# Kernel optimization log

Measured on AMD Instinct MI355X. Metric: run time of the kernel, lower is better.

## Reference

```python
import jax, jax.numpy as jnp
import numpy as np

N_NODES = 100000
N_EDGES = 1600000
F = 64          # node_features (in == out for EvolveGCNO)
HID = 64        # hidden_size


def setup_inputs() -> dict:
    key = jax.random.key(0)
    ks = jax.random.split(key, 12)
    s = 1.0 / np.sqrt(F)
    inp = {
        "x": jax.random.normal(ks[0], (N_NODES, F), dtype=jnp.float32),
        "edge_index": jax.random.randint(ks[1], (2, N_EDGES), 0, N_NODES, dtype=jnp.int64),
        "edge_weight": jax.random.uniform(ks[2], (N_EDGES,), dtype=jnp.float32),
        # evolving GCN weight (initial_weight of EvolveGCNO)
        "W0": jax.random.uniform(ks[3], (F, F), jnp.float32, -s, s),
        # GRU (input_size=F, hidden_size=F): gates ordered r, z, n
        "gru_Wi": jax.random.uniform(ks[4], (3 * F, F), jnp.float32, -s, s),
        "gru_Wh": jax.random.uniform(ks[5], (3 * F, F), jnp.float32, -s, s),
        "gru_bi": jax.random.uniform(ks[6], (3 * F,), jnp.float32, -s, s),
        "gru_bh": jax.random.uniform(ks[7], (3 * F,), jnp.float32, -s, s),
        # projection F -> HID and head HID -> 1
        "proj_W": jax.random.uniform(ks[8], (HID, F), jnp.float32, -s, s),
        "proj_b": jax.random.uniform(ks[9], (HID,), jnp.float32, -s, s),
        "lin_W": jax.random.uniform(ks[10], (1, HID), jnp.float32, -1.0 / np.sqrt(HID), 1.0 / np.sqrt(HID)),
        "lin_b": jax.random.uniform(ks[11], (1,), jnp.float32, -1.0 / np.sqrt(HID), 1.0 / np.sqrt(HID)),
    }
    return inp


def reference(x, edge_index, edge_weight, W0, gru_Wi, gru_Wh, gru_bi, gru_bh,
              proj_W, proj_b, lin_W, lin_b):
    N = x.shape[0]
    # --- EvolveGCNO weight evolution: one GRU step, rows of W0 are both input and hidden ---
    gi = W0 @ gru_Wi.T + gru_bi  # [F, 3F]
    gh = W0 @ gru_Wh.T + gru_bh  # [F, 3F]
    i_r, i_z, i_n = jnp.split(gi, 3, axis=1)
    h_r, h_z, h_n = jnp.split(gh, 3, axis=1)
    r = jax.nn.sigmoid(i_r + h_r)
    z = jax.nn.sigmoid(i_z + h_z)
    n = jnp.tanh(i_n + r * h_n)
    W = (1.0 - z) * n + z * W0  # evolved GCN weight [F, F]

    # --- GCNConv with fixed evolved W: X' = D^-1/2 (A + I) D^-1/2 (X W) ---
    xw = x @ W  # [N, F]
    src, dst = edge_index[0], edge_index[1]
    loop = jnp.arange(N)
    src2 = jnp.concatenate([src, loop])
    dst2 = jnp.concatenate([dst, loop])
    w2 = jnp.concatenate([edge_weight, jnp.ones((N,), xw.dtype)])  # self-loop weight 1
    deg = jax.ops.segment_sum(w2, dst2, num_segments=N)
    dinv = jnp.where(deg > 0, jax.lax.rsqrt(deg), 0.0)
    norm = dinv[src2] * w2 * dinv[dst2]  # [E + N]
    h = jax.ops.segment_sum(xw[src2] * norm[:, None], dst2, num_segments=N)  # [N, F]

    # --- MLP head (dropout is identity in eval) ---
    h = jax.nn.relu(h @ proj_W.T + proj_b)
    return h @ lin_W.T + lin_b  # [N, 1]
```

## Files before the change

kernel.cpp:

```cpp
#include <hip/hip_runtime.h>
#include <stdint.h>

#define FDIM 64
#define BINSH 6
#define NBINS 1563
#define BCAP 1536
#define OVCAP 8192
#define PSTAGE 8192
#define PBLK 196
#define LSTRIDE 72

__device__ __forceinline__ float bf2f(unsigned int u) {
    union { float f; uint32_t i; } v; v.i = (u & 0xFFFFu) << 16; return v.f;
}
__device__ __forceinline__ unsigned short f2bf(float f) {
    union { float f; uint32_t i; } v; v.f = f;
    uint32_t u = v.i;
    u += 0x7FFFu + ((u >> 16) & 1u);
    return (unsigned short)(u >> 16);
}

__global__ __launch_bounds__(256) void k_sentinel(float* out, int N, float val) {
    int n = blockIdx.x * 256 + threadIdx.x;
    if (n < N) out[n] = (n == 0) ? val : 0.f;
}

__global__ __launch_bounds__(1024) void k_prep(
    const int* __restrict__ src, const int* __restrict__ dst,
    const float* __restrict__ ew, int* __restrict__ gcnt,
    int2* __restrict__ part, int* __restrict__ ovf_cnt,
    int* __restrict__ ovs, int* __restrict__ ovd, float* __restrict__ ovw, int E,
    const float* __restrict__ W0, const float* __restrict__ Wi,
    const float* __restrict__ Wh, const float* __restrict__ bi,
    const float* __restrict__ bh, const float* __restrict__ projW,
    float* __restrict__ M) {
    __shared__ int2 sorted_[PSTAGE];
    __shared__ int  gposa[PSTAGE];
    __shared__ int  hist[NBINS];
    __shared__ int  lbase[NBINS];
    __shared__ int  lcur[NBINS];
    __shared__ int  gboff[NBINS];
    __shared__ int  wsum[16];
    int t = threadIdx.x;
    if (blockIdx.x < PBLK) {
        for (int b = t; b < NBINS; b += 1024) hist[b] = 0;
        __syncthreads();
        int e0 = blockIdx.x * PSTAGE;
        int cnt = E - e0; if (cnt > PSTAGE) cnt = PSTAGE;
        for (int i = t; i < cnt; i += 1024) atomicAdd(&hist[dst[e0 + i] >> BINSH], 1);
        __syncthreads();
        for (int b = t; b < NBINS; b += 1024) {
            int h = hist[b];
            gboff[b] = h ? atomicAdd(&gcnt[b], h) : 0;
        }
        int b0i = 2 * t, b1i = 2 * t + 1;
        int h0 = (b0i < NBINS) ? hist[b0i] : 0;
        int h1 = (b1i < NBINS) ? hist[b1i] : 0;
        int c2 = h0 + h1;
        int lane = t & 63, wid = t >> 6;
        int v = c2;
#pragma unroll
        for (int d = 1; d < 64; d <<= 1) {
            int o = __shfl_up(v, d);
            if (lane >= d) v += o;
        }
        if (lane == 63) wsum[wid] = v;
        __syncthreads();
        if (t < 16) {
            int w = wsum[t];
#pragma unroll
            for (int d = 1; d < 16; d <<= 1) {
                int o = __shfl_up(w, d);
                if (t >= d) w += o;
            }
            wsum[t] = w;
        }
        __syncthreads();
        int base = (wid > 0) ? wsum[wid - 1] : 0;
        int excl = base + v - c2;
        if (b0i < NBINS) { lbase[b0i] = excl;      lcur[b0i] = excl; }
        if (b1i < NBINS) { lbase[b1i] = excl + h0; lcur[b1i] = excl + h0; }
        __syncthreads();
        for (int i = t; i < cnt; i += 1024) {
            int e = e0 + i;
            int d = dst[e];
            int b = d >> BINSH;
            int p = atomicAdd(&lcur[b], 1);
            sorted_[p] = make_int2(src[e] | ((d & 63) << 20), __float_as_int(ew[e]));
            int off = gboff[b] + (p - lbase[b]);
            if (off < BCAP) {
                gposa[p] = b * BCAP + off;
            } else {
                gposa[p] = -1;
                int op = atomicAdd(ovf_cnt, 1);
                if (op < OVCAP) { ovs[op] = src[e]; ovd[op] = d; ovw[op] = ew[e]; }
            }
        }
        __syncthreads();
        for (int j = t; j < cnt; j += 1024) {
            int g = gposa[j];
            if (g >= 0) part[g] = sorted_[j];
        }
    } else {
        int i = blockIdx.x - PBLK;
        float* w0s  = (float*)sorted_;
        float* wrow = w0s + 64;
        if (t < 64) w0s[t] = W0[i * 64 + t];
        __syncthreads();
        if (t < 64) {
            int j = t;
            float a0 = 0.f, a1 = 0.f, a2 = 0.f, b0 = 0.f, b1 = 0.f, b2 = 0.f;
#pragma unroll 8
            for (int k = 0; k < 64; k++) {
                float w0k = w0s[k];
                a0 += w0k * Wi[(j)       * 64 + k];
                a1 += w0k * Wi[(64 + j)  * 64 + k];
                a2 += w0k * Wi[(128 + j) * 64 + k];
                b0 += w0k * Wh[(j)       * 64 + k];
                b1 += w0k * Wh[(64 + j)  * 64 + k];
                b2 += w0k * Wh[(128 + j) * 64 + k];
            }
            float ir = a0 + bi[j],        hr = b0 + bh[j];
            float iz = a1 + bi[64 + j],   hz = b1 + bh[64 + j];
            float in_ = a2 + bi[128 + j], hn = b2 + bh[128 + j];
            float r = 1.f / (1.f + expf(-(ir + hr)));
            float z = 1.f / (1.f + expf(-(iz + hz)));
            float n = tanhf(in_ + r * hn);
            wrow[j] = (1.f - z) * n + z * w0s[j];
        }
        __syncthreads();
        if (t < 64) {
            float s = 0.f;
#pragma unroll 8
            for (int q = 0; q < 64; q++) s += wrow[q] * projW[t * 64 + q];
            M[i * 64 + t] = s;
        }
    }
}

__global__ __launch_bounds__(256) void k_xmdeg(
    const float* __restrict__ x, const float* __restrict__ M,
    unsigned short* __restrict__ xm, int N,
    const int* __restrict__ gcnt, const int2* __restrict__ part,
    const int* __restrict__ ovf_cnt, const int* __restrict__ ovd,
    const float* __restrict__ ovw, float* __restrict__ dinv,
    int* __restrict__ loffg) {
    __shared__ char sm[34816];
    int t = threadIdx.x;
    if (blockIdx.x < NBINS) {
        float* xs = (float*)sm;
        float* ms = xs + 64 * 68;
        int nb = blockIdx.x * 64;
#pragma unroll
        for (int i = 0; i < 4; i++) {
            int lin = i * 1024 + t * 4;
            int row = lin >> 6, col = lin & 63;
            int node = nb + row;
            float4 v = make_float4(0.f, 0.f, 0.f, 0.f);
            if (node < N) v = *(const float4*)(x + (size_t)node * 64 + col);
            *(float4*)&xs[row * 68 + col] = v;
            *(float4*)&ms[row * 68 + col] = *(const float4*)(M + lin);
        }
        __syncthreads();
        int tj = t & 15, tn = t >> 4;
        float acc[4][4] = {};
        for (int k = 0; k < 64; k += 4) {
            float4 xv[4], mv[4];
#pragma unroll
            for (int nn = 0; nn < 4; nn++) xv[nn] = *(const float4*)&xs[(tn * 4 + nn) * 68 + k];
#pragma unroll
            for (int kk = 0; kk < 4; kk++) mv[kk] = *(const float4*)&ms[(k + kk) * 68 + tj * 4];
#pragma unroll
            for (int nn = 0; nn < 4; nn++) {
                const float* xp = (const float*)&xv[nn];
#pragma unroll
                for (int kk = 0; kk < 4; kk++) {
                    float xk = xp[kk];
                    const float* mp = (const float*)&mv[kk];
                    acc[nn][0] += xk * mp[0];
                    acc[nn][1] += xk * mp[1];
                    acc[nn][2] += xk * mp[2];
                    acc[nn][3] += xk * mp[3];
                }
            }
        }
#pragma unroll
        for (int nn = 0; nn < 4; nn++) {
            int node = nb + tn * 4 + nn;
            if (node < N) {
                ushort4 o;
                o.x = f2bf(acc[nn][0]); o.y = f2bf(acc[nn][1]);
                o.z = f2bf(acc[nn][2]); o.w = f2bf(acc[nn][3]);
                *(ushort4*)&xm[(size_t)node * 64 + tj * 4] = o;
            }
        }
    } else {
        int b = blockIdx.x - NBINS;
        float* dl   = (float*)sm;
        int*   cntl = (int*)(dl + 64);
        int*   lofl = cntl + 64;
        if (t < 64) { dl[t] = 1.0f; cntl[t] = 0; }
        __syncthreads();
        int c = gcnt[b]; if (c > BCAP) c = BCAP;
        const int2* pe = part + (size_t)b * BCAP;
        for (int i = t; i < c; i += 256) {
            int2 e = pe[i];
            int nl = (e.x >> 20) & 63;
            atomicAdd(&dl[nl], __int_as_float(e.y));
            atomicAdd(&cntl[nl], 1);
        }
        int m = *ovf_cnt; if (m > OVCAP) m = OVCAP;
        for (int i = t; i < m; i += 256) {
            int d = ovd[i];
            if ((d >> BINSH) == b) atomicAdd(&dl[d & 63], ovw[i]);
        }
        __syncthreads();
        if (t == 0) {
            int o = 0;
#pragma unroll 16
            for (int k = 0; k < 64; k++) { lofl[k] = o; o += cntl[k]; }
            lofl[64] = o;
        }
        __syncthreads();
        if (t < 64) {
            int n = b * 64 + t;
            if (n < N) dinv[n] = rsqrtf(dl[t]);
        }
        if (t < 65) loffg[b * LSTRIDE + t] = lofl[t];
    }
}

__global__ __launch_bounds__(256) void k_gf(
    const unsigned short* __restrict__ xm, const float* __restrict__ dinv,
    const int* __restrict__ gcnt, const int2* __restrict__ part,
    const int* __restrict__ loffg,
    const float* __restrict__ projB, const float* __restrict__ linW,
    const float* __restrict__ linB, const int* __restrict__ ovf_cnt,
    const int* __restrict__ ovs, const int* __restrict__ ovd,
    const float* __restrict__ ovw, float* __restrict__ out, int N) {
    __shared__ int  loff[65];
    __shared__ int  lcur[32];
    __shared__ int2 ledge[BCAP];
    __shared__ float pbs[64], lws[64];
    int t = threadIdx.x, hb = blockIdx.x;
    int b = hb >> 1, half = hb & 1, nl0 = half << 5;
    if (t < 65) loff[t] = loffg[b * LSTRIDE + t];
    if (t < 64) { pbs[t] = projB[t]; lws[t] = linW[t]; }
    __syncthreads();
    int base = loff[nl0];
    if (t < 32) lcur[t] = loff[nl0 + t] - base;
    __syncthreads();
    int c = gcnt[b]; if (c > BCAP) c = BCAP;
    const int2* pe = part + (size_t)b * BCAP;
    for (int i = t; i < c; i += 256) {
        int2 e = pe[i];
        int nl = (e.x >> 20) & 63;
        if ((nl >> 5) != half) continue;
        int s = e.x & 0xFFFFF;
        float nw = dinv[s] * __int_as_float(e.y);
        int p = atomicAdd(&lcur[nl & 31], 1);
        ledge[p] = make_int2(e.x, __float_as_int(nw));
    }
    __syncthreads();
    int m = *ovf_cnt; if (m > OVCAP) m = OVCAP;
    float lb = linB[0];
    int wv = t >> 6, lane = t & 63, eg = lane >> 4, fq = lane & 15, f = fq * 4;
    for (int j = wv; j < 32; j += 4) {
        int nl = nl0 + j;
        int n = b * 64 + nl;
        if (n >= N) continue;
        float dn = dinv[n];
        int beg = loff[nl] - base, end = loff[nl + 1] - base;
        float a0 = 0.f, a1 = 0.f, a2 = 0.f, a3 = 0.f;
        float b0 = 0.f, b1 = 0.f, b2 = 0.f, b3 = 0.f;
        float c0 = 0.f, c1 = 0.f, c2 = 0.f, c3 = 0.f;
        float d0 = 0.f, d1 = 0.f, d2 = 0.f, d3 = 0.f;
        int i = beg + eg;
        for (; i + 12 < end; i += 16) {
            int2 e0 = ledge[i];
            int2 e1 = ledge[i + 4];
            int2 e2 = ledge[i + 8];
            int2 e3 = ledge[i + 12];
            uint2 u0 = *(const uint2*)&xm[(size_t)(e0.x & 0xFFFFF) * 64 + f];
            uint2 u1 = *(const uint2*)&xm[(size_t)(e1.x & 0xFFFFF) * 64 + f];
            uint2 u2 = *(const uint2*)&xm[(size_t)(e2.x & 0xFFFFF) * 64 + f];
            uint2 u3 = *(const uint2*)&xm[(size_t)(e3.x & 0xFFFFF) * 64 + f];
            float w0 = __int_as_float(e0.y);
            float w1 = __int_as_float(e1.y);
            float w2 = __int_as_float(e2.y);
            float w3 = __int_as_float(e3.y);
            a0 += w0 * bf2f(u0.x); a1 += w0 * bf2f(u0.x >> 16);
            a2 += w0 * bf2f(u0.y); a3 += w0 * bf2f(u0.y >> 16);
            b0 += w1 * bf2f(u1.x); b1 += w1 * bf2f(u1.x >> 16);
            b2 += w1 * bf2f(u1.y); b3 += w1 * bf2f(u1.y >> 16);
            c0 += w2 * bf2f(u2.x); c1 += w2 * bf2f(u2.x >> 16);
            c2 += w2 * bf2f(u2.y); c3 += w2 * bf2f(u2.y >> 16);
            d0 += w3 * bf2f(u3.x); d1 += w3 * bf2f(u3.x >> 16);
            d2 += w3 * bf2f(u3.y); d3 += w3 * bf2f(u3.y >> 16);
        }
        for (; i + 4 < end; i += 8) {
            int2 e0 = ledge[i];
            int2 e1 = ledge[i + 4];
            uint2 u0 = *(const uint2*)&xm[(size_t)(e0.x & 0xFFFFF) * 64 + f];
            uint2 u1 = *(const uint2*)&xm[(size_t)(e1.x & 0xFFFFF) * 64 + f];
            float w0 = __int_as_float(e0.y);
            float w1 = __int_as_float(e1.y);
            a0 += w0 * bf2f(u0.x); a1 += w0 * bf2f(u0.x >> 16);
            a2 += w0 * bf2f(u0.y); a3 += w0 * bf2f(u0.y >> 16);
            b0 += w1 * bf2f(u1.x); b1 += w1 * bf2f(u1.x >> 16);
            b2 += w1 * bf2f(u1.y); b3 += w1 * bf2f(u1.y >> 16);
        }
        for (; i < end; i += 4) {
            int2 e0 = ledge[i];
            uint2 u0 = *(const uint2*)&xm[(size_t)(e0.x & 0xFFFFF) * 64 + f];
            float w0 = __int_as_float(e0.y);
            a0 += w0 * bf2f(u0.x); a1 += w0 * bf2f(u0.x >> 16);
            a2 += w0 * bf2f(u0.y); a3 += w0 * bf2f(u0.y >> 16);
        }
        a0 += b0 + c0 + d0; a1 += b1 + c1 + d1;
        a2 += b2 + c2 + d2; a3 += b3 + c3 + d3;
        a0 *= dn; a1 *= dn; a2 *= dn; a3 *= dn;
        a0 += __shfl_xor(a0, 16); a1 += __shfl_xor(a1, 16);
        a2 += __shfl_xor(a2, 16); a3 += __shfl_xor(a3, 16);
        a0 += __shfl_xor(a0, 32); a1 += __shfl_xor(a1, 32);
        a2 += __shfl_xor(a2, 32); a3 += __shfl_xor(a3, 32);
        if (eg == 0) {
            {
                uint2 u = *(const uint2*)&xm[(size_t)n * 64 + f];
                float sl = dn * dn;
                a0 += sl * bf2f(u.x); a1 += sl * bf2f(u.x >> 16);
                a2 += sl * bf2f(u.y); a3 += sl * bf2f(u.y >> 16);
            }
            for (int q = 0; q < m; q++) {
                if (ovd[q] == n) {
                    int s = ovs[q];
                    float nm = dinv[s] * ovw[q] * dn;
                    uint2 u = *(const uint2*)&xm[(size_t)s * 64 + f];
                    a0 += nm * bf2f(u.x); a1 += nm * bf2f(u.x >> 16);
                    a2 += nm * bf2f(u.y); a3 += nm * bf2f(u.y >> 16);
                }
            }
            float v0 = a0 + pbs[f],     v1 = a1 + pbs[f + 1];
            float v2 = a2 + pbs[f + 2], v3 = a3 + pbs[f + 3];
            float s = (v0 > 0.f ? v0 : 0.f) * lws[f]
                    + (v1 > 0.f ? v1 : 0.f) * lws[f + 1]
                    + (v2 > 0.f ? v2 : 0.f) * lws[f + 2]
                    + (v3 > 0.f ? v3 : 0.f) * lws[f + 3];
            s += __shfl_xor(s, 1); s += __shfl_xor(s, 2);
            s += __shfl_xor(s, 4); s += __shfl_xor(s, 8);
            if (fq == 0) out[n] = s + lb;
        }
    }
}

extern "C" void kernel_launch(void* const* d_in, const int* in_sizes, int n_in,
                              void* d_out, int out_size, void* d_ws, size_t ws_size,
                              hipStream_t stream) {
    const float* x   = (const float*)d_in[0];
    const int*   ei  = (const int*)d_in[1];
    const float* ew  = (const float*)d_in[2];
    const float* W0  = (const float*)d_in[3];
    const float* gWi = (const float*)d_in[4];
    const float* gWh = (const float*)d_in[5];
    const float* gbi = (const float*)d_in[6];
    const float* gbh = (const float*)d_in[7];
    const float* pW  = (const float*)d_in[8];
    const float* pb  = (const float*)d_in[9];
    const float* lW  = (const float*)d_in[10];
    const float* lb  = (const float*)d_in[11];
    float* out = (float*)d_out;

    static const int EXPSZ[12] = {6400000, 3200000, 1600000, 4096, 12288, 12288,
                                  192, 192, 4096, 64, 64, 1};
    int mism = -1;
    for (int i = 0; i < 12 && i < n_in; i++)
        if (in_sizes[i] != EXPSZ[i]) { mism = i; break; }
    if (mism >= 0) {
        k_sentinel<<<(out_size + 255) / 256, 256, 0, stream>>>(out, out_size,
                                                               ldexpf(1.f, 30 + 3 * mism));
        return;
    }

    int N = in_sizes[0] / FDIM;
    int E = in_sizes[1] / 2;
    const int* src = ei;
    const int* dst = ei + E;

    char* wsb = (char*)d_ws;
    float* M       = (float*)(wsb);
    int*   gcnt    = (int*)  (wsb + (32u << 10));
    int*   ovf_cnt = (int*)  (wsb + (39u << 10));
    int*   ovs     = (int*)  (wsb + (44u << 10));
    int*   ovd     = (int*)  (wsb + (76u << 10));
    float* ovw     = (float*)(wsb + (108u << 10));
    float* dinv    = (float*)(wsb + (1u << 20));
    int*   loffg   = (int*)  (wsb + 1572864u);
    int2*  part    = (int2*) (wsb + (2u << 20));
    unsigned short* xm = (unsigned short*)(wsb + (22u << 20));

    hipMemsetAsync(gcnt, 0, (8u << 10), stream);

    k_prep<<<PBLK + 64, 1024, 0, stream>>>(src, dst, ew, gcnt, part,
                                           ovf_cnt, ovs, ovd, ovw, E,
                                           W0, gWi, gWh, gbi, gbh, pW, M);
    k_xmdeg<<<NBINS * 2, 256, 0, stream>>>(x, M, xm, N, gcnt, part,
                                           ovf_cnt, ovd, ovw, dinv, loffg);
    k_gf<<<NBINS * 2, 256, 0, stream>>>(xm, dinv, gcnt, part, loffg, pb, lW, lb,
                                        ovf_cnt, ovs, ovd, ovw, out, N);
}
```

Baseline: 188.9 us.

## Split GRU into own kernel and co-schedule x@M GEMM with edge partitioning

Moves the GRU weight-evolution work into a small standalone kernel that runs first. The x@M bf16 GEMM then runs as extra 1024-thread blocks (four 64-node tiles each) inside the edge-partitioning kernel, so the compute-bound GEMM overlaps the memory- and atomic-heavy binning. Degree and offset computation moves into its own kernel. This trades one extra launch and a large shared-memory union, which limits occupancy, for overlapping two independent phases.

```diff
diff --git a/kernel.cpp b/kernel.cpp
--- a/kernel.cpp
+++ b/kernel.cpp
@@ -8,6 +8,7 @@
 #define OVCAP 8192
 #define PSTAGE 8192
 #define PBLK 196
+#define GBLK 391
 #define LSTRIDE 72
 
 __device__ __forceinline__ float bf2f(unsigned int u) {
@@ -25,24 +26,63 @@
     if (n < N) out[n] = (n == 0) ? val : 0.f;
 }
 
-__global__ __launch_bounds__(1024) void k_prep(
+__global__ __launch_bounds__(64) void k_gru(
+    const float* __restrict__ W0, const float* __restrict__ Wi,
+    const float* __restrict__ Wh, const float* __restrict__ bi,
+    const float* __restrict__ bh, const float* __restrict__ projW,
+    float* __restrict__ M) {
+    __shared__ float w0s[64];
+    __shared__ float wrow[64];
+    int i = blockIdx.x, t = threadIdx.x;
+    w0s[t] = W0[i * 64 + t];
+    __syncthreads();
+    {
+        int j = t;
+        float a0 = 0.f, a1 = 0.f, a2 = 0.f, b0 = 0.f, b1 = 0.f, b2 = 0.f;
+#pragma unroll 8
+        for (int k = 0; k < 64; k++) {
+            float w0k = w0s[k];
+            a0 += w0k * Wi[(j)       * 64 + k];
+            a1 += w0k * Wi[(64 + j)  * 64 + k];
+            a2 += w0k * Wi[(128 + j) * 64 + k];
+            b0 += w0k * Wh[(j)       * 64 + k];
+            b1 += w0k * Wh[(64 + j)  * 64 + k];
+            b2 += w0k * Wh[(128 + j) * 64 + k];
+        }
+        float ir = a0 + bi[j],        hr = b0 + bh[j];
+        float iz = a1 + bi[64 + j],   hz = b1 + bh[64 + j];
+        float in_ = a2 + bi[128 + j], hn = b2 + bh[128 + j];
+        float r = 1.f / (1.f + expf(-(ir + hr)));
+        float z = 1.f / (1.f + expf(-(iz + hz)));
+        float n = tanhf(in_ + r * hn);
+        wrow[j] = (1.f - z) * n + z * w0s[j];
+    }
+    __syncthreads();
+    {
+        float s = 0.f;
+#pragma unroll 8
+        for (int q = 0; q < 64; q++) s += wrow[q] * projW[t * 64 + q];
+        M[i * 64 + t] = s;
+    }
+}
+
+__global__ __launch_bounds__(1024) void k_pg(
     const int* __restrict__ src, const int* __restrict__ dst,
     const float* __restrict__ ew, int* __restrict__ gcnt,
     int2* __restrict__ part, int* __restrict__ ovf_cnt,
     int* __restrict__ ovs, int* __restrict__ ovd, float* __restrict__ ovw, int E,
-    const float* __restrict__ W0, const float* __restrict__ Wi,
-    const float* __restrict__ Wh, const float* __restrict__ bi,
-    const float* __restrict__ bh, const float* __restrict__ projW,
-    float* __restrict__ M) {
-    __shared__ int2 sorted_[PSTAGE];
-    __shared__ int  gposa[PSTAGE];
-    __shared__ int  hist[NBINS];
-    __shared__ int  lbase[NBINS];
-    __shared__ int  lcur[NBINS];
-    __shared__ int  gboff[NBINS];
-    __shared__ int  wsum[16];
+    const float* __restrict__ x, const float* __restrict__ M,
+    unsigned short* __restrict__ xm, int N) {
+    __shared__ __align__(16) char smu[123456];
     int t = threadIdx.x;
     if (blockIdx.x < PBLK) {
+        int2* sorted_ = (int2*)smu;
+        int*  gposa   = (int*)(smu + 65536);
+        int*  hist    = (int*)(smu + 98304);
+        int*  lbase   = (int*)(smu + 98304 + 6256);
+        int*  lcur    = (int*)(smu + 98304 + 12512);
+        int*  gboff   = (int*)(smu + 98304 + 18768);
+        int*  wsum    = (int*)(smu + 98304 + 25024);
         for (int b = t; b < NBINS; b += 1024) hist[b] = 0;
         __syncthreads();
         int e0 = blockIdx.x * PSTAGE;
@@ -102,67 +142,26 @@
             if (g >= 0) part[g] = sorted_[j];
         }
     } else {
-        int i = blockIdx.x - PBLK;
-        float* w0s  = (float*)sorted_;
-        float* wrow = w0s + 64;
-        if (t < 64) w0s[t] = W0[i * 64 + t];
-        __syncthreads();
-        if (t < 64) {
-            int j = t;
-            float a0 = 0.f, a1 = 0.f, a2 = 0.f, b0 = 0.f, b1 = 0.f, b2 = 0.f;
-#pragma unroll 8
-            for (int k = 0; k < 64; k++) {
-                float w0k = w0s[k];
-                a0 += w0k * Wi[(j)       * 64 + k];
-                a1 += w0k * Wi[(64 + j)  * 64 + k];
-                a2 += w0k * Wi[(128 + j) * 64 + k];
-                b0 += w0k * Wh[(j)       * 64 + k];
-                b1 += w0k * Wh[(64 + j)  * 64 + k];
-                b2 += w0k * Wh[(128 + j) * 64 + k];
-            }
-            float ir = a0 + bi[j],        hr = b0 + bh[j];
-            float iz = a1 + bi[64 + j],   hz = b1 + bh[64 + j];
-            float in_ = a2 + bi[128 + j], hn = b2 + bh[128 + j];
-            float r = 1.f / (1.f + expf(-(ir + hr)));
-            float z = 1.f / (1.f + expf(-(iz + hz)));
-            float n = tanhf(in_ + r * hn);
-            wrow[j] = (1.f - z) * n + z * w0s[j];
-        }
-        __syncthreads();
-        if (t < 64) {
-            float s = 0.f;
-#pragma unroll 8
-            for (int q = 0; q < 64; q++) s += wrow[q] * projW[t * 64 + q];
-            M[i * 64 + t] = s;
-        }
-    }
-}
-
-__global__ __launch_bounds__(256) void k_xmdeg(
-    const float* __restrict__ x, const float* __restrict__ M,
-    unsigned short* __restrict__ xm, int N,
-    const int* __restrict__ gcnt, const int2* __restrict__ part,
-    const int* __restrict__ ovf_cnt, const int* __restrict__ ovd,
-    const float* __restrict__ ovw, float* __restrict__ dinv,
-    int* __restrict__ loffg) {
-    __shared__ char sm[34816];
-    int t = threadIdx.x;
-    if (blockIdx.x < NBINS) {
-        float* xs = (float*)sm;
-        float* ms = xs + 64 * 68;
-        int nb = blockIdx.x * 64;
+        int g = t >> 8, tt = t & 255;
+        int tile = (blockIdx.x - PBLK) * 4 + g;
+        float* ms = (float*)smu;
+        float* xs = (float*)(smu + 17408 + g * 17408);
+        {
+            int lin = t * 4;
+            *(float4*)&ms[(lin >> 6) * 68 + (lin & 63)] = *(const float4*)(M + lin);
+        }
+        int nb = tile * 64;
 #pragma unroll
         for (int i = 0; i < 4; i++) {
-            int lin = i * 1024 + t * 4;
+            int lin = i * 1024 + tt * 4;
             int row = lin >> 6, col = lin & 63;
             int node = nb + row;
             float4 v = make_float4(0.f, 0.f, 0.f, 0.f);
             if (node < N) v = *(const float4*)(x + (size_t)node * 64 + col);
             *(float4*)&xs[row * 68 + col] = v;
-            *(float4*)&ms[row * 68 + col] = *(const float4*)(M + lin);
-        }
-        __syncthreads();
-        int tj = t & 15, tn = t >> 4;
+        }
+        __syncthreads();
+        int tj = tt & 15, tn = tt >> 4;
         float acc[4][4] = {};
         for (int k = 0; k < 64; k += 4) {
             float4 xv[4], mv[4];
@@ -194,40 +193,46 @@
                 *(ushort4*)&xm[(size_t)node * 64 + tj * 4] = o;
             }
         }
-    } else {
-        int b = blockIdx.x - NBINS;
-        float* dl   = (float*)sm;
-        int*   cntl = (int*)(dl + 64);
-        int*   lofl = cntl + 64;
-        if (t < 64) { dl[t] = 1.0f; cntl[t] = 0; }
-        __syncthreads();
-        int c = gcnt[b]; if (c > BCAP) c = BCAP;
-        const int2* pe = part + (size_t)b * BCAP;
-        for (int i = t; i < c; i += 256) {
-            int2 e = pe[i];
-            int nl = (e.x >> 20) & 63;
-            atomicAdd(&dl[nl], __int_as_float(e.y));
-            atomicAdd(&cntl[nl], 1);
-        }
-        int m = *ovf_cnt; if (m > OVCAP) m = OVCAP;
-        for (int i = t; i < m; i += 256) {
-            int d = ovd[i];
-            if ((d >> BINSH) == b) atomicAdd(&dl[d & 63], ovw[i]);
-        }
-        __syncthreads();
-        if (t == 0) {
-            int o = 0;
+    }
+}
+
+__global__ __launch_bounds__(256) void k_deg(
+    const int* __restrict__ gcnt, const int2* __restrict__ part,
+    const int* __restrict__ ovf_cnt, const int* __restrict__ ovd,
+    const float* __restrict__ ovw, float* __restrict__ dinv,
+    int* __restrict__ loffg, int N) {
+    __shared__ float dl[64];
+    __shared__ int   cntl[64];
+    __shared__ int   lofl[65];
+    int t = threadIdx.x, b = blockIdx.x;
+    if (t < 64) { dl[t] = 1.0f; cntl[t] = 0; }
+    __syncthreads();
+    int c = gcnt[b]; if (c > BCAP) c = BCAP;
+    const int2* pe = part + (size_t)b * BCAP;
+    for (int i = t; i < c; i += 256) {
+        int2 e = pe[i];
+        int nl = (e.x >> 20) & 63;
+        atomicAdd(&dl[nl], __int_as_float(e.y));
+        atomicAdd(&cntl[nl], 1);
+    }
+    int m = *ovf_cnt; if (m > OVCAP) m = OVCAP;
+    for (int i = t; i < m; i += 256) {
+        int d = ovd[i];
+        if ((d >> BINSH) == b) atomicAdd(&dl[d & 63], ovw[i]);
+    }
+    __syncthreads();
+    if (t == 0) {
+        int o = 0;
 #pragma unroll 16
-            for (int k = 0; k < 64; k++) { lofl[k] = o; o += cntl[k]; }
-            lofl[64] = o;
-        }
-        __syncthreads();
-        if (t < 64) {
-            int n = b * 64 + t;
-            if (n < N) dinv[n] = rsqrtf(dl[t]);
-        }
-        if (t < 65) loffg[b * LSTRIDE + t] = lofl[t];
-    }
+        for (int k = 0; k < 64; k++) { lofl[k] = o; o += cntl[k]; }
+        lofl[64] = o;
+    }
+    __syncthreads();
+    if (t < 64) {
+        int n = b * 64 + t;
+        if (n < N) dinv[n] = rsqrtf(dl[t]);
+    }
+    if (t < 65) loffg[b * LSTRIDE + t] = lofl[t];
 }
 
 __global__ __launch_bounds__(256) void k_gf(
@@ -400,11 +405,12 @@
 
     hipMemsetAsync(gcnt, 0, (8u << 10), stream);
 
-    k_prep<<<PBLK + 64, 1024, 0, stream>>>(src, dst, ew, gcnt, part,
+    k_gru<<<64, 64, 0, stream>>>(W0, gWi, gWh, gbi, gbh, pW, M);
+    k_pg<<<PBLK + GBLK, 1024, 0, stream>>>(src, dst, ew, gcnt, part,
                                            ovf_cnt, ovs, ovd, ovw, E,
-                                           W0, gWi, gWh, gbi, gbh, pW, M);
-    k_xmdeg<<<NBINS * 2, 256, 0, stream>>>(x, M, xm, N, gcnt, part,
-                                           ovf_cnt, ovd, ovw, dinv, loffg);
+                                           x, M, xm, N);
+    k_deg<<<NBINS, 256, 0, stream>>>(gcnt, part, ovf_cnt, ovd, ovw,
+                                     dinv, loffg, N);
     k_gf<<<NBINS * 2, 256, 0, stream>>>(xm, dinv, gcnt, part, loffg, pb, lW, lb,
                                         ovf_cnt, ovs, ovd, ovw, out, N);
 }
```

New measurement: 196.6 us. 4.1% more time.
